# Kernel tuning notes

Hardware: AMD Instinct MI355X
Metric: run time of the kernel (lower is better)

## Reference

```python
import jax, jax.numpy as jnp
import numpy as np

N = 50000      # nodes (cells)
E = 800000     # directed edges
IN, H1, H2, Z = 512, 128, 128, 64


def setup_inputs() -> dict:
    key = jax.random.key(0)
    ks = jax.random.split(key, 12)
    x = jax.random.normal(ks[0], (N, IN), jnp.float32)
    edge_index = jax.random.randint(ks[1], (2, E), 0, N, dtype=jnp.int64)

    def glorot(k, i, o):
        return jax.random.normal(k, (i, o), jnp.float32) * np.float32(1.0 / np.sqrt(i))

    return {
        "x": x,
        "edge_index": edge_index,
        "W1": glorot(ks[2], IN, H1), "b1": jnp.zeros((H1,), jnp.float32),
        "W2": glorot(ks[3], H1, H2), "b2": jnp.zeros((H2,), jnp.float32),
        "Wm": glorot(ks[4], H2, Z),  "bm": jnp.zeros((Z,), jnp.float32),
        "Ws": glorot(ks[5], H2, Z),  "bs": jnp.zeros((Z,), jnp.float32),
    }


def _gcn_norm(edge_index, n):
    # PyG GCNConv default: add self-loops, sym-normalize D^-1/2 (A+I) D^-1/2
    loops = jnp.arange(n, dtype=edge_index.dtype)
    src = jnp.concatenate([edge_index[0], loops])
    dst = jnp.concatenate([edge_index[1], loops])
    deg = jax.ops.segment_sum(jnp.ones_like(dst, jnp.float32), dst, num_segments=n)
    dis = jnp.where(deg > 0, jax.lax.rsqrt(jnp.maximum(deg, 1.0)), 0.0)
    norm = dis[src] * dis[dst]  # [E+N]
    return src, dst, norm


def _gcn_conv(x, W, b, src, dst, norm, n):
    h = x @ W                          # [N, out] transform first
    msg = h[src] * norm[:, None]       # gather + scale
    out = jax.ops.segment_sum(msg, dst, num_segments=n)  # scatter-add at targets
    return out + b


def reference(x, edge_index, W1, b1, W2, b2, Wm, bm, Ws, bs):
    n = x.shape[0]
    src, dst, norm = _gcn_norm(edge_index, n)
    h = jax.nn.relu(_gcn_conv(x, W1, b1, src, dst, norm, n))
    h = jax.nn.relu(_gcn_conv(h, W2, b2, src, dst, norm, n))
    # dropout p=0.4 is identity in eval mode
    z_mean = _gcn_conv(h, Wm, bm, src, dst, norm, n)
    z_log_std = _gcn_conv(h, Ws, bs, src, dst, norm, n)
    return (z_mean, z_log_std)
```

## Files before the change

kernel.cpp:

```cpp
#include <hip/hip_runtime.h>


using u16 = unsigned short;
typedef __attribute__((ext_vector_type(8))) short short8;
typedef __attribute__((ext_vector_type(4))) float f32x4;

__device__ __forceinline__ void split_bf16(float f, u16& hi, u16& lo) {
    unsigned b = __float_as_uint(f);
    hi = (u16)(b >> 16);
    float rem = f - __uint_as_float(b & 0xFFFF0000u);
    lo = (u16)(__float_as_uint(rem) >> 16);
}

__device__ __forceinline__ int block_mode(const int* __restrict__ ew, int* sflag) {
    if (threadIdx.x == 0) *sflag = 0;
    __syncthreads();
    if (ew[2 * (int)threadIdx.x + 1] != 0) atomicOr(sflag, 1);
    __syncthreads();
    return *sflag ? 0 : 1;
}

__global__ void deg_kernel(const int* __restrict__ ew, int* __restrict__ deg, int E) {
    __shared__ int sflag;
    int mode = block_mode(ew, &sflag);
    int e = blockIdx.x * blockDim.x + threadIdx.x;
    if (e >= E) return;
    int d = mode ? ew[2 * E + 2 * e] : ew[E + e];
    atomicAdd(&deg[d], 1);
}

__global__ void scan_block_kernel(const int* __restrict__ deg, int* __restrict__ rowptr,
                                  int* __restrict__ aux, float* __restrict__ dis, int N) {
    __shared__ int s[256];
    int i = blockIdx.x * 256 + threadIdx.x;
    int v = (i < N) ? deg[i] : 0;
    if (i < N) dis[i] = rsqrtf((float)v + 1.0f);
    s[threadIdx.x] = v;
    __syncthreads();
    for (int off = 1; off < 256; off <<= 1) {
        int t = (threadIdx.x >= off) ? s[threadIdx.x - off] : 0;
        __syncthreads();
        s[threadIdx.x] += t;
        __syncthreads();
    }
    if (i < N) rowptr[i] = s[threadIdx.x] - v;
    if (threadIdx.x == 255) aux[blockIdx.x] = s[255];
}

__global__ void scan_aux_kernel(int* __restrict__ aux, int nb) {
    __shared__ int s[256];
    int i = threadIdx.x;
    int v = (i < nb) ? aux[i] : 0;
    s[i] = v;
    __syncthreads();
    for (int off = 1; off < 256; off <<= 1) {
        int t = (i >= off) ? s[i - off] : 0;
        __syncthreads();
        s[i] += t;
        __syncthreads();
    }
    if (i < nb) aux[i] = s[i] - v;
}

__global__ void add_offsets_kernel(int* __restrict__ rowptr, const int* __restrict__ aux,
                                   int* __restrict__ cursor, int N, int E) {
    int i = blockIdx.x * 256 + threadIdx.x;
    if (i < N) {
        int rp = rowptr[i] + aux[i >> 8];
        rowptr[i] = rp;
        cursor[i] = rp;
    }
    if (i == 0) rowptr[N] = E;
}

__global__ void fill_csr_kernel(const int* __restrict__ ew,
                                int* __restrict__ cursor,
                                int* __restrict__ csr_src, int E) {
    __shared__ int sflag;
    int mode = block_mode(ew, &sflag);
    int e = blockIdx.x * blockDim.x + threadIdx.x;
    if (e >= E) return;
    int s = mode ? ew[2 * e] : ew[e];
    int d = mode ? ew[2 * E + 2 * e] : ew[E + e];
    int pos = atomicAdd(&cursor[d], 1);
    csr_src[pos] = s;
}

__global__ void conv_all_kernel(const float* __restrict__ W1, const float* __restrict__ W2,
                                const float* __restrict__ Wm, const float* __restrict__ Ws,
                                u16* __restrict__ B1h, u16* __restrict__ B1l,
                                u16* __restrict__ B2h, u16* __restrict__ B2l,
                                u16* __restrict__ Bch, u16* __restrict__ Bcl) {
    int idx = blockIdx.x * 256 + threadIdx.x;
    u16 h, l;
    if (idx < 65536) {
        int t = idx >> 13;
        int ks = (idx >> 9) & 15;
        int L = (idx >> 3) & 63;
        int q = idx & 7;
        int col = t * 16 + (L & 15);
        int k = ks * 32 + (L >> 4) * 8 + q;
        split_bf16(W1[k * 128 + col], h, l);
        B1h[idx] = h;
        B1l[idx] = l;
    } else if (idx < 81920) {
        int o = idx - 65536;
        int t = o >> 11;
        int ks = (o >> 9) & 3;
        int L = (o >> 3) & 63;
        int q = o & 7;
        int col = t * 16 + (L & 15);
        int k = ks * 32 + (L >> 4) * 8 + q;
        split_bf16(W2[k * 128 + col], h, l);
        B2h[o] = h;
        B2l[o] = l;
    } else if (idx < 98304) {
        int o = idx - 81920;
        int t = o >> 11;
        int ks = (o >> 9) & 3;
        int L = (o >> 3) & 63;
        int q = o & 7;
        int col = t * 16 + (L & 15);
        int k = ks * 32 + (L >> 4) * 8 + q;
        float f = (col < 64) ? Wm[k * 64 + col] : Ws[k * 64 + (col - 64)];
        split_bf16(f, h, l);
        Bch[o] = h;
        Bcl[o] = l;
    }
}

#define TILE_OFF(t) ((t) * 520)

__global__ __launch_bounds__(256) void gemm_mfma(const float* __restrict__ A,
                                                 const u16* __restrict__ Bfh,
                                                 const u16* __restrict__ Bfl,
                                                 const float* __restrict__ dis,
                                                 float* __restrict__ C,
                                                 int N, int K) {
    __shared__ __align__(16) u16 AsH[4 * 520], AsL[4 * 520];

    const int tid = threadIdx.x;
    const int w = tid >> 6, lane = tid & 63;
    const int m16 = lane & 15, quad = lane >> 4;
    const int row0 = blockIdx.x * 64;

    const int s_ar = w * 16 + (lane & 15);
    const int s_ak = (lane >> 4) * 8;
    const int a_dst = TILE_OFF(w) + lane * 8;

    const int R = (w >> 1) * 32, Cc = (w & 1) * 64;
    const int atile = (w >> 1) * 2;
    const int btile = (w & 1) * 4;

    const int ksteps = K >> 5;
    const u16* bfh = Bfh + ((size_t)btile * ksteps) * 512 + lane * 8;
    const u16* bfl = Bfl + ((size_t)btile * ksteps) * 512 + lane * 8;

    f32x4 acc[2][4];
#pragma unroll
    for (int i = 0; i < 2; ++i)
#pragma unroll
        for (int j = 0; j < 4; ++j) acc[i][j] = (f32x4)0.f;

    float dr[2][4];
#pragma unroll
    for (int i = 0; i < 2; ++i)
#pragma unroll
        for (int r = 0; r < 4; ++r) {
            int gr = row0 + R + i * 16 + quad * 4 + r;
            dr[i][r] = dis[gr < N ? gr : N - 1];
        }

    const int grow = row0 + s_ar;
    const bool ok = (grow < N);
    const float* aptr = A + (size_t)grow * K + s_ak;

    float av[8];
    {
        f32x4 v0 = (f32x4)0.f, v1 = (f32x4)0.f;
        if (ok) { v0 = *(const f32x4*)&aptr[0]; v1 = *(const f32x4*)&aptr[4]; }
#pragma unroll
        for (int q = 0; q < 4; ++q) { av[q] = v0[q]; av[4 + q] = v1[q]; }
    }

    for (int ks = 0; ks < ksteps; ++ks) {
        short8 fbh[4], fbl[4];
#pragma unroll
        for (int j = 0; j < 4; ++j) {
            fbh[j] = *(const short8*)(bfh + (size_t)(j * ksteps + ks) * 512);
            fbl[j] = *(const short8*)(bfl + (size_t)(j * ksteps + ks) * 512);
        }

        short8 ah, al;
#pragma unroll
        for (int q = 0; q < 8; ++q) {
            u16 h, l;
            split_bf16(av[q], h, l);
            ah[q] = (short)h;
            al[q] = (short)l;
        }
        __syncthreads();
        *(short8*)&AsH[a_dst] = ah;
        *(short8*)&AsL[a_dst] = al;
        __syncthreads();

        if (ks + 1 < ksteps) {
            const int k0 = (ks + 1) * 32;
            f32x4 v0 = (f32x4)0.f, v1 = (f32x4)0.f;
            if (ok) { v0 = *(const f32x4*)&aptr[k0]; v1 = *(const f32x4*)&aptr[k0 + 4]; }
#pragma unroll
            for (int q = 0; q < 4; ++q) { av[q] = v0[q]; av[4 + q] = v1[q]; }
        }

        short8 fah[2], fal[2];
#pragma unroll
        for (int i = 0; i < 2; ++i) {
            fah[i] = *(const short8*)&AsH[TILE_OFF(atile + i) + lane * 8];
            fal[i] = *(const short8*)&AsL[TILE_OFF(atile + i) + lane * 8];
        }

#pragma unroll
        for (int i = 0; i < 2; ++i)
#pragma unroll
            for (int j = 0; j < 4; ++j) {
                acc[i][j] = __builtin_amdgcn_mfma_f32_16x16x32_bf16(
                    fah[i], fbh[j], acc[i][j], 0, 0, 0);
                acc[i][j] = __builtin_amdgcn_mfma_f32_16x16x32_bf16(
                    fah[i], fbl[j], acc[i][j], 0, 0, 0);
                acc[i][j] = __builtin_amdgcn_mfma_f32_16x16x32_bf16(
                    fal[i], fbh[j], acc[i][j], 0, 0, 0);
            }
    }

#pragma unroll
    for (int i = 0; i < 2; ++i) {
#pragma unroll
        for (int r = 0; r < 4; ++r) {
            int gr = row0 + R + i * 16 + quad * 4 + r;
            if (gr < N) {
#pragma unroll
                for (int j = 0; j < 4; ++j)
                    C[(size_t)gr * 128 + Cc + j * 16 + m16] = acc[i][j][r] * dr[i][r];
            }
        }
    }
}

__global__ __launch_bounds__(256) void propagate_kernel(
    const float* __restrict__ hs, const int* __restrict__ rowptr,
    const int* __restrict__ csr_src, const float* __restrict__ dis,
    const float* __restrict__ bias, float* __restrict__ out, int N, int do_relu) {
    int wave = (blockIdx.x * 256 + threadIdx.x) >> 6;
    int lane = threadIdx.x & 63;
    if (wave >= N) return;
    const int v = wave;
    const int half = lane >> 5, c = lane & 31;
    const int f4 = c * 4;
    const float dv = dis[v];
    f32x4 acc = (f32x4)0.f;
    const int beg = rowptr[v], end = rowptr[v + 1];
    int i = beg;
    for (; i + 8 <= end; i += 8) {
        int s[4];
        f32x4 g[4];
#pragma unroll
        for (int u = 0; u < 4; ++u) s[u] = csr_src[i + 2 * u + half];
#pragma unroll
        for (int u = 0; u < 4; ++u) g[u] = *(const f32x4*)&hs[(size_t)s[u] * 128 + f4];
#pragma unroll
        for (int u = 0; u < 4; ++u) acc += g[u];
    }
    for (; i + 2 <= end; i += 2) {
        int s = csr_src[i + half];
        acc += *(const f32x4*)&hs[(size_t)s * 128 + f4];
    }
    if (i < end && half == 0) {
        int s = csr_src[i];
        acc += *(const f32x4*)&hs[(size_t)s * 128 + f4];
    }
#pragma unroll
    for (int k = 0; k < 4; ++k) acc[k] += __shfl_xor(acc[k], 32);
    if (half == 0) {
        const f32x4 hv = *(const f32x4*)&hs[(size_t)v * 128 + f4];
        const f32x4 b = *(const f32x4*)&bias[f4];
        f32x4 o;
#pragma unroll
        for (int k = 0; k < 4; ++k) {
            float t = dv * (acc[k] + hv[k]) + b[k];
            o[k] = do_relu ? fmaxf(t, 0.f) : t;
        }
        *(f32x4*)&out[(size_t)v * 128 + f4] = o;
    }
}

__global__ void __launch_bounds__(256) propagate_final_kernel(
    const float* __restrict__ hs, const int* __restrict__ rowptr,
    const int* __restrict__ csr_src, const float* __restrict__ dis,
    const float* __restrict__ bm, const float* __restrict__ bs,
    float* __restrict__ out, int N) {
    int wave = (blockIdx.x * 256 + threadIdx.x) >> 6;
    int lane = threadIdx.x & 63;
    if (wave >= N) return;
    const int v = wave;
    const int half = lane >> 5, c = lane & 31;
    const int f4 = c * 4;
    const float dv = dis[v];
    f32x4 acc = (f32x4)0.f;
    const int beg = rowptr[v], end = rowptr[v + 1];
    int i = beg;
    for (; i + 8 <= end; i += 8) {
        int s[4];
        f32x4 g[4];
#pragma unroll
        for (int u = 0; u < 4; ++u) s[u] = csr_src[i + 2 * u + half];
#pragma unroll
        for (int u = 0; u < 4; ++u) g[u] = *(const f32x4*)&hs[(size_t)s[u] * 128 + f4];
#pragma unroll
        for (int u = 0; u < 4; ++u) acc += g[u];
    }
    for (; i + 2 <= end; i += 2) {
        int s = csr_src[i + half];
        acc += *(const f32x4*)&hs[(size_t)s * 128 + f4];
    }
    if (i < end && half == 0) {
        int s = csr_src[i];
        acc += *(const f32x4*)&hs[(size_t)s * 128 + f4];
    }
#pragma unroll
    for (int k = 0; k < 4; ++k) acc[k] += __shfl_xor(acc[k], 32);
    if (half == 0) {
        const f32x4 hv = *(const f32x4*)&hs[(size_t)v * 128 + f4];
        f32x4 o;
        if (f4 < 64) {
            const f32x4 b = *(const f32x4*)&bm[f4];
#pragma unroll
            for (int k = 0; k < 4; ++k) o[k] = dv * (acc[k] + hv[k]) + b[k];
            *(f32x4*)&out[(size_t)v * 64 + f4] = o;
        } else {
            const int g = f4 - 64;
            const f32x4 b = *(const f32x4*)&bs[g];
#pragma unroll
            for (int k = 0; k < 4; ++k) o[k] = dv * (acc[k] + hv[k]) + b[k];
            *(f32x4*)&out[(size_t)N * 64 + (size_t)v * 64 + g] = o;
        }
    }
}

extern "C" void kernel_launch(void* const* d_in, const int* in_sizes, int n_in,
                              void* d_out, int out_size, void* d_ws, size_t ws_size,
                              hipStream_t stream) {
    const float* x  = (const float*)d_in[0];
    const int*   ew = (const int*)d_in[1];
    const float* W1 = (const float*)d_in[2];
    const float* b1 = (const float*)d_in[3];
    const float* W2 = (const float*)d_in[4];
    const float* b2 = (const float*)d_in[5];
    const float* Wm = (const float*)d_in[6];
    const float* bm = (const float*)d_in[7];
    const float* Ws = (const float*)d_in[8];
    const float* bs = (const float*)d_in[9];
    float* out = (float*)d_out;

    const int IN = 512, H = 128;
    const int N = in_sizes[0] / IN;
    const int E = in_sizes[1] / 2;

    char* base = (char*)d_ws;
    size_t off = 0;
    auto alloc = [&](size_t bytes) -> char* {
        char* p = base + off;
        off = (off + bytes + 255) & ~(size_t)255;
        return p;
    };
    int*   deg     = (int*)  alloc((size_t)N * 4);
    int*   cursor  = (int*)  alloc((size_t)N * 4);
    float* dis     = (float*)alloc((size_t)N * 4);
    int*   rowptr  = (int*)  alloc((size_t)(N + 1) * 4);
    int*   aux     = (int*)  alloc(256 * 4);
    int*   csr_src = (int*)  alloc((size_t)E * 4);
    u16*   B1h     = (u16*)  alloc((size_t)IN * H * 2);
    u16*   B1l     = (u16*)  alloc((size_t)IN * H * 2);
    u16*   B2h     = (u16*)  alloc((size_t)H * H * 2);
    u16*   B2l     = (u16*)  alloc((size_t)H * H * 2);
    u16*   Bch     = (u16*)  alloc((size_t)H * H * 2);
    u16*   Bcl     = (u16*)  alloc((size_t)H * H * 2);
    float* hA      = (float*)alloc((size_t)N * H * 4);
    float* hB      = (float*)alloc((size_t)N * H * 4);
    (void)ws_size; (void)n_in; (void)out_size;

    hipMemsetAsync(deg, 0, (size_t)N * 4, stream);

    const int eblocks = (E + 255) / 256;
    const int nblocks = (N + 255) / 256;

    conv_all_kernel<<<(98304 + 255) / 256, 256, 0, stream>>>(
        W1, W2, Wm, Ws, B1h, B1l, B2h, B2l, Bch, Bcl);
    deg_kernel<<<eblocks, 256, 0, stream>>>(ew, deg, E);
    scan_block_kernel<<<nblocks, 256, 0, stream>>>(deg, rowptr, aux, dis, N);
    scan_aux_kernel<<<1, 256, 0, stream>>>(aux, nblocks);
    add_offsets_kernel<<<nblocks, 256, 0, stream>>>(rowptr, aux, cursor, N, E);
    fill_csr_kernel<<<eblocks, 256, 0, stream>>>(ew, cursor, csr_src, E);

    const int gblocks = (N + 63) / 64;
    const int pblocks = (N * 64 + 255) / 256;

    gemm_mfma<<<gblocks, 256, 0, stream>>>(x, B1h, B1l, dis, hA, N, IN);
    propagate_kernel<<<pblocks, 256, 0, stream>>>(hA, rowptr, csr_src, dis,
                                                  b1, hB, N, 1);
    gemm_mfma<<<gblocks, 256, 0, stream>>>(hB, B2h, B2l, dis, hA, N, H);
    propagate_kernel<<<pblocks, 256, 0, stream>>>(hA, rowptr, csr_src, dis,
                                                  b2, hB, N, 1);
    gemm_mfma<<<gblocks, 256, 0, stream>>>(hB, Bch, Bcl, dis, hA, N, H);
    propagate_final_kernel<<<pblocks, 256, 0, stream>>>(hA, rowptr, csr_src, dis,
                                                        bm, bs, out, N);
}
```

Measured before the change: 488.0 us.

## Fuse all stages into one persistent kernel with software grid barriers

Replaces the chain of eleven kernel launches (weight conversion, degree count, scans, CSR fill, three GEMMs, three propagations) with one persistent kernel of 768 blocks. The stages are separated by an atomic counter and generation grid barrier, and the work is spread with grid-stride loops. This removes per-launch overhead and the idle gaps between kernels. In exchange it relies on all 768 blocks being resident at once (launch_bounds 256,3), otherwise the barrier deadlocks. It also adds spin-wait barrier cost and may cut per-stage occupancy and parallelism compared with the full-size grids.

```diff
diff --git a/kernel.cpp b/kernel.cpp
--- a/kernel.cpp
+++ b/kernel.cpp
@@ -12,137 +12,33 @@
     lo = (u16)(__float_as_uint(rem) >> 16);
 }
 
-__device__ __forceinline__ int block_mode(const int* __restrict__ ew, int* sflag) {
-    if (threadIdx.x == 0) *sflag = 0;
+#define TILE_OFF(t) ((t) * 520)
+
+__device__ __forceinline__ void gbar(int* cnt, int* gen, int nb) {
     __syncthreads();
-    if (ew[2 * (int)threadIdx.x + 1] != 0) atomicOr(sflag, 1);
+    if (threadIdx.x == 0) {
+        __threadfence();
+        int g = atomicAdd(gen, 0);
+        if (atomicAdd(cnt, 1) == nb - 1) {
+            atomicExch(cnt, 0);
+            atomicAdd(gen, 1);
+        } else {
+            while (atomicAdd(gen, 0) == g) __builtin_amdgcn_s_sleep(2);
+        }
+        __threadfence();
+    }
     __syncthreads();
-    return *sflag ? 0 : 1;
-}
-
-__global__ void deg_kernel(const int* __restrict__ ew, int* __restrict__ deg, int E) {
-    __shared__ int sflag;
-    int mode = block_mode(ew, &sflag);
-    int e = blockIdx.x * blockDim.x + threadIdx.x;
-    if (e >= E) return;
-    int d = mode ? ew[2 * E + 2 * e] : ew[E + e];
-    atomicAdd(&deg[d], 1);
-}
-
-__global__ void scan_block_kernel(const int* __restrict__ deg, int* __restrict__ rowptr,
-                                  int* __restrict__ aux, float* __restrict__ dis, int N) {
-    __shared__ int s[256];
-    int i = blockIdx.x * 256 + threadIdx.x;
-    int v = (i < N) ? deg[i] : 0;
-    if (i < N) dis[i] = rsqrtf((float)v + 1.0f);
-    s[threadIdx.x] = v;
-    __syncthreads();
-    for (int off = 1; off < 256; off <<= 1) {
-        int t = (threadIdx.x >= off) ? s[threadIdx.x - off] : 0;
-        __syncthreads();
-        s[threadIdx.x] += t;
-        __syncthreads();
-    }
-    if (i < N) rowptr[i] = s[threadIdx.x] - v;
-    if (threadIdx.x == 255) aux[blockIdx.x] = s[255];
-}
-
-__global__ void scan_aux_kernel(int* __restrict__ aux, int nb) {
-    __shared__ int s[256];
-    int i = threadIdx.x;
-    int v = (i < nb) ? aux[i] : 0;
-    s[i] = v;
-    __syncthreads();
-    for (int off = 1; off < 256; off <<= 1) {
-        int t = (i >= off) ? s[i - off] : 0;
-        __syncthreads();
-        s[i] += t;
-        __syncthreads();
-    }
-    if (i < nb) aux[i] = s[i] - v;
-}
-
-__global__ void add_offsets_kernel(int* __restrict__ rowptr, const int* __restrict__ aux,
-                                   int* __restrict__ cursor, int N, int E) {
-    int i = blockIdx.x * 256 + threadIdx.x;
-    if (i < N) {
-        int rp = rowptr[i] + aux[i >> 8];
-        rowptr[i] = rp;
-        cursor[i] = rp;
-    }
-    if (i == 0) rowptr[N] = E;
-}
-
-__global__ void fill_csr_kernel(const int* __restrict__ ew,
-                                int* __restrict__ cursor,
-                                int* __restrict__ csr_src, int E) {
-    __shared__ int sflag;
-    int mode = block_mode(ew, &sflag);
-    int e = blockIdx.x * blockDim.x + threadIdx.x;
-    if (e >= E) return;
-    int s = mode ? ew[2 * e] : ew[e];
-    int d = mode ? ew[2 * E + 2 * e] : ew[E + e];
-    int pos = atomicAdd(&cursor[d], 1);
-    csr_src[pos] = s;
-}
-
-__global__ void conv_all_kernel(const float* __restrict__ W1, const float* __restrict__ W2,
-                                const float* __restrict__ Wm, const float* __restrict__ Ws,
-                                u16* __restrict__ B1h, u16* __restrict__ B1l,
-                                u16* __restrict__ B2h, u16* __restrict__ B2l,
-                                u16* __restrict__ Bch, u16* __restrict__ Bcl) {
-    int idx = blockIdx.x * 256 + threadIdx.x;
-    u16 h, l;
-    if (idx < 65536) {
-        int t = idx >> 13;
-        int ks = (idx >> 9) & 15;
-        int L = (idx >> 3) & 63;
-        int q = idx & 7;
-        int col = t * 16 + (L & 15);
-        int k = ks * 32 + (L >> 4) * 8 + q;
-        split_bf16(W1[k * 128 + col], h, l);
-        B1h[idx] = h;
-        B1l[idx] = l;
-    } else if (idx < 81920) {
-        int o = idx - 65536;
-        int t = o >> 11;
-        int ks = (o >> 9) & 3;
-        int L = (o >> 3) & 63;
-        int q = o & 7;
-        int col = t * 16 + (L & 15);
-        int k = ks * 32 + (L >> 4) * 8 + q;
-        split_bf16(W2[k * 128 + col], h, l);
-        B2h[o] = h;
-        B2l[o] = l;
-    } else if (idx < 98304) {
-        int o = idx - 81920;
-        int t = o >> 11;
-        int ks = (o >> 9) & 3;
-        int L = (o >> 3) & 63;
-        int q = o & 7;
-        int col = t * 16 + (L & 15);
-        int k = ks * 32 + (L >> 4) * 8 + q;
-        float f = (col < 64) ? Wm[k * 64 + col] : Ws[k * 64 + (col - 64)];
-        split_bf16(f, h, l);
-        Bch[o] = h;
-        Bcl[o] = l;
-    }
-}
-
-#define TILE_OFF(t) ((t) * 520)
-
-__global__ __launch_bounds__(256) void gemm_mfma(const float* __restrict__ A,
-                                                 const u16* __restrict__ Bfh,
-                                                 const u16* __restrict__ Bfl,
-                                                 const float* __restrict__ dis,
-                                                 float* __restrict__ C,
-                                                 int N, int K) {
-    __shared__ __align__(16) u16 AsH[4 * 520], AsL[4 * 520];
-
+}
+
+__device__ __forceinline__ void gemm_tile(
+    const float* __restrict__ A, const u16* __restrict__ Bfh,
+    const u16* __restrict__ Bfl, const float* __restrict__ dis,
+    float* __restrict__ C, int N, int K, int tile,
+    u16* AsH, u16* AsL) {
     const int tid = threadIdx.x;
     const int w = tid >> 6, lane = tid & 63;
     const int m16 = lane & 15, quad = lane >> 4;
-    const int row0 = blockIdx.x * 64;
+    const int row0 = tile * 64;
 
     const int s_ar = w * 16 + (lane & 15);
     const int s_ak = (lane >> 4) * 8;
@@ -246,104 +142,239 @@
     }
 }
 
-__global__ __launch_bounds__(256) void propagate_kernel(
+__device__ __forceinline__ void prop_std(
     const float* __restrict__ hs, const int* __restrict__ rowptr,
     const int* __restrict__ csr_src, const float* __restrict__ dis,
-    const float* __restrict__ bias, float* __restrict__ out, int N, int do_relu) {
-    int wave = (blockIdx.x * 256 + threadIdx.x) >> 6;
-    int lane = threadIdx.x & 63;
-    if (wave >= N) return;
-    const int v = wave;
+    const float* __restrict__ bias, float* __restrict__ o, int N,
+    int do_relu, int nwaves) {
+    const int lane = threadIdx.x & 63;
     const int half = lane >> 5, c = lane & 31;
     const int f4 = c * 4;
-    const float dv = dis[v];
-    f32x4 acc = (f32x4)0.f;
-    const int beg = rowptr[v], end = rowptr[v + 1];
-    int i = beg;
-    for (; i + 8 <= end; i += 8) {
-        int s[4];
-        f32x4 g[4];
-#pragma unroll
-        for (int u = 0; u < 4; ++u) s[u] = csr_src[i + 2 * u + half];
-#pragma unroll
-        for (int u = 0; u < 4; ++u) g[u] = *(const f32x4*)&hs[(size_t)s[u] * 128 + f4];
-#pragma unroll
-        for (int u = 0; u < 4; ++u) acc += g[u];
-    }
-    for (; i + 2 <= end; i += 2) {
-        int s = csr_src[i + half];
-        acc += *(const f32x4*)&hs[(size_t)s * 128 + f4];
-    }
-    if (i < end && half == 0) {
-        int s = csr_src[i];
-        acc += *(const f32x4*)&hs[(size_t)s * 128 + f4];
-    }
-#pragma unroll
-    for (int k = 0; k < 4; ++k) acc[k] += __shfl_xor(acc[k], 32);
-    if (half == 0) {
-        const f32x4 hv = *(const f32x4*)&hs[(size_t)v * 128 + f4];
-        const f32x4 b = *(const f32x4*)&bias[f4];
-        f32x4 o;
-#pragma unroll
-        for (int k = 0; k < 4; ++k) {
-            float t = dv * (acc[k] + hv[k]) + b[k];
-            o[k] = do_relu ? fmaxf(t, 0.f) : t;
-        }
-        *(f32x4*)&out[(size_t)v * 128 + f4] = o;
-    }
-}
-
-__global__ void __launch_bounds__(256) propagate_final_kernel(
+    const int w0 = ((int)blockIdx.x * 256 + (int)threadIdx.x) >> 6;
+    for (int v = w0; v < N; v += nwaves) {
+        const float dv = dis[v];
+        f32x4 acc = (f32x4)0.f;
+        const int beg = rowptr[v], end = rowptr[v + 1];
+        int i = beg;
+        for (; i + 8 <= end; i += 8) {
+            int s[4];
+            f32x4 g[4];
+#pragma unroll
+            for (int u = 0; u < 4; ++u) s[u] = csr_src[i + 2 * u + half];
+#pragma unroll
+            for (int u = 0; u < 4; ++u) g[u] = *(const f32x4*)&hs[(size_t)s[u] * 128 + f4];
+#pragma unroll
+            for (int u = 0; u < 4; ++u) acc += g[u];
+        }
+        for (; i + 2 <= end; i += 2) {
+            int s = csr_src[i + half];
+            acc += *(const f32x4*)&hs[(size_t)s * 128 + f4];
+        }
+        if (i < end && half == 0) {
+            int s = csr_src[i];
+            acc += *(const f32x4*)&hs[(size_t)s * 128 + f4];
+        }
+#pragma unroll
+        for (int k = 0; k < 4; ++k) acc[k] += __shfl_xor(acc[k], 32);
+        if (half == 0) {
+            const f32x4 hv = *(const f32x4*)&hs[(size_t)v * 128 + f4];
+            const f32x4 b = *(const f32x4*)&bias[f4];
+            f32x4 oo;
+#pragma unroll
+            for (int k = 0; k < 4; ++k) {
+                float t = dv * (acc[k] + hv[k]) + b[k];
+                oo[k] = do_relu ? fmaxf(t, 0.f) : t;
+            }
+            *(f32x4*)&o[(size_t)v * 128 + f4] = oo;
+        }
+    }
+}
+
+__device__ __forceinline__ void prop_fin(
     const float* __restrict__ hs, const int* __restrict__ rowptr,
     const int* __restrict__ csr_src, const float* __restrict__ dis,
     const float* __restrict__ bm, const float* __restrict__ bs,
-    float* __restrict__ out, int N) {
-    int wave = (blockIdx.x * 256 + threadIdx.x) >> 6;
-    int lane = threadIdx.x & 63;
-    if (wave >= N) return;
-    const int v = wave;
+    float* __restrict__ o, int N, int nwaves) {
+    const int lane = threadIdx.x & 63;
     const int half = lane >> 5, c = lane & 31;
     const int f4 = c * 4;
-    const float dv = dis[v];
-    f32x4 acc = (f32x4)0.f;
-    const int beg = rowptr[v], end = rowptr[v + 1];
-    int i = beg;
-    for (; i + 8 <= end; i += 8) {
-        int s[4];
-        f32x4 g[4];
-#pragma unroll
-        for (int u = 0; u < 4; ++u) s[u] = csr_src[i + 2 * u + half];
-#pragma unroll
-        for (int u = 0; u < 4; ++u) g[u] = *(const f32x4*)&hs[(size_t)s[u] * 128 + f4];
-#pragma unroll
-        for (int u = 0; u < 4; ++u) acc += g[u];
-    }
-    for (; i + 2 <= end; i += 2) {
-        int s = csr_src[i + half];
-        acc += *(const f32x4*)&hs[(size_t)s * 128 + f4];
-    }
-    if (i < end && half == 0) {
-        int s = csr_src[i];
-        acc += *(const f32x4*)&hs[(size_t)s * 128 + f4];
-    }
-#pragma unroll
-    for (int k = 0; k < 4; ++k) acc[k] += __shfl_xor(acc[k], 32);
-    if (half == 0) {
-        const f32x4 hv = *(const f32x4*)&hs[(size_t)v * 128 + f4];
-        f32x4 o;
-        if (f4 < 64) {
-            const f32x4 b = *(const f32x4*)&bm[f4];
-#pragma unroll
-            for (int k = 0; k < 4; ++k) o[k] = dv * (acc[k] + hv[k]) + b[k];
-            *(f32x4*)&out[(size_t)v * 64 + f4] = o;
+    const int w0 = ((int)blockIdx.x * 256 + (int)threadIdx.x) >> 6;
+    for (int v = w0; v < N; v += nwaves) {
+        const float dv = dis[v];
+        f32x4 acc = (f32x4)0.f;
+        const int beg = rowptr[v], end = rowptr[v + 1];
+        int i = beg;
+        for (; i + 8 <= end; i += 8) {
+            int s[4];
+            f32x4 g[4];
+#pragma unroll
+            for (int u = 0; u < 4; ++u) s[u] = csr_src[i + 2 * u + half];
+#pragma unroll
+            for (int u = 0; u < 4; ++u) g[u] = *(const f32x4*)&hs[(size_t)s[u] * 128 + f4];
+#pragma unroll
+            for (int u = 0; u < 4; ++u) acc += g[u];
+        }
+        for (; i + 2 <= end; i += 2) {
+            int s = csr_src[i + half];
+            acc += *(const f32x4*)&hs[(size_t)s * 128 + f4];
+        }
+        if (i < end && half == 0) {
+            int s = csr_src[i];
+            acc += *(const f32x4*)&hs[(size_t)s * 128 + f4];
+        }
+#pragma unroll
+        for (int k = 0; k < 4; ++k) acc[k] += __shfl_xor(acc[k], 32);
+        if (half == 0) {
+            const f32x4 hv = *(const f32x4*)&hs[(size_t)v * 128 + f4];
+            f32x4 oo;
+            if (f4 < 64) {
+                const f32x4 b = *(const f32x4*)&bm[f4];
+#pragma unroll
+                for (int k = 0; k < 4; ++k) oo[k] = dv * (acc[k] + hv[k]) + b[k];
+                *(f32x4*)&o[(size_t)v * 64 + f4] = oo;
+            } else {
+                const int g = f4 - 64;
+                const f32x4 b = *(const f32x4*)&bs[g];
+#pragma unroll
+                for (int k = 0; k < 4; ++k) oo[k] = dv * (acc[k] + hv[k]) + b[k];
+                *(f32x4*)&o[(size_t)N * 64 + (size_t)v * 64 + g] = oo;
+            }
+        }
+    }
+}
+
+__global__ __launch_bounds__(256, 3) void fused_all(
+    const float* __restrict__ x, const int* __restrict__ ew,
+    const float* __restrict__ W1, const float* __restrict__ b1,
+    const float* __restrict__ W2, const float* __restrict__ b2,
+    const float* __restrict__ Wm, const float* __restrict__ bm,
+    const float* __restrict__ Ws, const float* __restrict__ bs,
+    int* cnt, int* gen, int* deg, int* cursor, float* dis,
+    int* rowptr, int* aux, int* csr_src,
+    u16* B1h, u16* B1l, u16* B2h, u16* B2l, u16* Bch, u16* Bcl,
+    float* hA, float* hB, float* out, int N, int E) {
+    __shared__ __align__(16) u16 AsH[4 * 520], AsL[4 * 520];
+    __shared__ int sint[257];
+
+    const int tid = threadIdx.x;
+    const int bid = blockIdx.x;
+    const int NB = gridDim.x;
+    const int gtid = bid * 256 + tid;
+    const int GT = NB * 256;
+    const int nwaves = NB * 4;
+
+    int mode;
+    {
+        if (tid == 0) sint[256] = 0;
+        __syncthreads();
+        if (ew[2 * tid + 1] != 0) atomicOr(&sint[256], 1);
+        __syncthreads();
+        mode = sint[256] ? 0 : 1;
+        __syncthreads();
+    }
+
+    if (gtid < 98304) {
+        int idx = gtid;
+        u16 h, l;
+        if (idx < 65536) {
+            int t = idx >> 13, ks = (idx >> 9) & 15, L = (idx >> 3) & 63, q = idx & 7;
+            int col = t * 16 + (L & 15);
+            int k = ks * 32 + (L >> 4) * 8 + q;
+            split_bf16(W1[k * 128 + col], h, l);
+            B1h[idx] = h; B1l[idx] = l;
+        } else if (idx < 81920) {
+            int o = idx - 65536;
+            int t = o >> 11, ks = (o >> 9) & 3, L = (o >> 3) & 63, q = o & 7;
+            int col = t * 16 + (L & 15);
+            int k = ks * 32 + (L >> 4) * 8 + q;
+            split_bf16(W2[k * 128 + col], h, l);
+            B2h[o] = h; B2l[o] = l;
         } else {
-            const int g = f4 - 64;
-            const f32x4 b = *(const f32x4*)&bs[g];
-#pragma unroll
-            for (int k = 0; k < 4; ++k) o[k] = dv * (acc[k] + hv[k]) + b[k];
-            *(f32x4*)&out[(size_t)N * 64 + (size_t)v * 64 + g] = o;
-        }
-    }
+            int o = idx - 81920;
+            int t = o >> 11, ks = (o >> 9) & 3, L = (o >> 3) & 63, q = o & 7;
+            int col = t * 16 + (L & 15);
+            int k = ks * 32 + (L >> 4) * 8 + q;
+            float f = (col < 64) ? Wm[k * 64 + col] : Ws[k * 64 + (col - 64)];
+            split_bf16(f, h, l);
+            Bch[o] = h; Bcl[o] = l;
+        }
+    }
+    for (int e = gtid; e < E; e += GT) {
+        int d = mode ? ew[2 * E + 2 * e] : ew[E + e];
+        atomicAdd(&deg[d], 1);
+    }
+    gbar(cnt, gen, NB);
+
+    const int nch = (N + 255) >> 8;
+    for (int ch = bid; ch < nch; ch += NB) {
+        int i = ch * 256 + tid;
+        int v = (i < N) ? deg[i] : 0;
+        if (i < N) dis[i] = rsqrtf((float)v + 1.0f);
+        sint[tid] = v;
+        __syncthreads();
+        for (int off = 1; off < 256; off <<= 1) {
+            int t = (tid >= off) ? sint[tid - off] : 0;
+            __syncthreads();
+            sint[tid] += t;
+            __syncthreads();
+        }
+        if (i < N) rowptr[i] = sint[tid] - v;
+        if (tid == 255) aux[ch] = sint[255];
+        __syncthreads();
+    }
+    gbar(cnt, gen, NB);
+
+    if (bid == 0) {
+        int v = (tid < nch) ? aux[tid] : 0;
+        sint[tid] = v;
+        __syncthreads();
+        for (int off = 1; off < 256; off <<= 1) {
+            int t = (tid >= off) ? sint[tid - off] : 0;
+            __syncthreads();
+            sint[tid] += t;
+            __syncthreads();
+        }
+        if (tid < nch) aux[tid] = sint[tid] - v;
+    }
+    gbar(cnt, gen, NB);
+
+    for (int i = gtid; i < N; i += GT) {
+        int rp = rowptr[i] + aux[i >> 8];
+        rowptr[i] = rp;
+        cursor[i] = rp;
+    }
+    if (gtid == 0) rowptr[N] = E;
+    gbar(cnt, gen, NB);
+
+    for (int e = gtid; e < E; e += GT) {
+        int s = mode ? ew[2 * e] : ew[e];
+        int d = mode ? ew[2 * E + 2 * e] : ew[E + e];
+        int pos = atomicAdd(&cursor[d], 1);
+        csr_src[pos] = s;
+    }
+    gbar(cnt, gen, NB);
+
+    const int ntiles = (N + 63) >> 6;
+
+    for (int t = bid; t < ntiles; t += NB)
+        gemm_tile(x, B1h, B1l, dis, hA, N, 512, t, AsH, AsL);
+    gbar(cnt, gen, NB);
+
+    prop_std(hA, rowptr, csr_src, dis, b1, hB, N, 1, nwaves);
+    gbar(cnt, gen, NB);
+
+    for (int t = bid; t < ntiles; t += NB)
+        gemm_tile(hB, B2h, B2l, dis, hA, N, 128, t, AsH, AsL);
+    gbar(cnt, gen, NB);
+
+    prop_std(hA, rowptr, csr_src, dis, b2, hB, N, 1, nwaves);
+    gbar(cnt, gen, NB);
+
+    for (int t = bid; t < ntiles; t += NB)
+        gemm_tile(hB, Bch, Bcl, dis, hA, N, 128, t, AsH, AsL);
+    gbar(cnt, gen, NB);
+
+    prop_fin(hA, rowptr, csr_src, dis, bm, bs, out, N, nwaves);
 }
 
 extern "C" void kernel_launch(void* const* d_in, const int* in_sizes, int n_in,
@@ -372,6 +403,7 @@
         off = (off + bytes + 255) & ~(size_t)255;
         return p;
     };
+    int*   sync2   = (int*)  alloc(256);
     int*   deg     = (int*)  alloc((size_t)N * 4);
     int*   cursor  = (int*)  alloc((size_t)N * 4);
     float* dis     = (float*)alloc((size_t)N * 4);
@@ -388,29 +420,11 @@
     float* hB      = (float*)alloc((size_t)N * H * 4);
     (void)ws_size; (void)n_in; (void)out_size;
 
-    hipMemsetAsync(deg, 0, (size_t)N * 4, stream);
-
-    const int eblocks = (E + 255) / 256;
-    const int nblocks = (N + 255) / 256;
-
-    conv_all_kernel<<<(98304 + 255) / 256, 256, 0, stream>>>(
-        W1, W2, Wm, Ws, B1h, B1l, B2h, B2l, Bch, Bcl);
-    deg_kernel<<<eblocks, 256, 0, stream>>>(ew, deg, E);
-    scan_block_kernel<<<nblocks, 256, 0, stream>>>(deg, rowptr, aux, dis, N);
-    scan_aux_kernel<<<1, 256, 0, stream>>>(aux, nblocks);
-    add_offsets_kernel<<<nblocks, 256, 0, stream>>>(rowptr, aux, cursor, N, E);
-    fill_csr_kernel<<<eblocks, 256, 0, stream>>>(ew, cursor, csr_src, E);
-
-    const int gblocks = (N + 63) / 64;
-    const int pblocks = (N * 64 + 255) / 256;
-
-    gemm_mfma<<<gblocks, 256, 0, stream>>>(x, B1h, B1l, dis, hA, N, IN);
-    propagate_kernel<<<pblocks, 256, 0, stream>>>(hA, rowptr, csr_src, dis,
-                                                  b1, hB, N, 1);
-    gemm_mfma<<<gblocks, 256, 0, stream>>>(hB, B2h, B2l, dis, hA, N, H);
-    propagate_kernel<<<pblocks, 256, 0, stream>>>(hA, rowptr, csr_src, dis,
-                                                  b2, hB, N, 1);
-    gemm_mfma<<<gblocks, 256, 0, stream>>>(hB, Bch, Bcl, dis, hA, N, H);
-    propagate_final_kernel<<<pblocks, 256, 0, stream>>>(hA, rowptr, csr_src, dis,
-                                                        bm, bs, out, N);
-}
+    size_t zlen = (size_t)((char*)cursor - (char*)sync2);
+    hipMemsetAsync(sync2, 0, zlen, stream);
+
+    fused_all<<<768, 256, 0, stream>>>(
+        x, ew, W1, b1, W2, b2, Wm, bm, Ws, bs,
+        &sync2[0], &sync2[1], deg, cursor, dis, rowptr, aux, csr_src,
+        B1h, B1l, B2h, B2l, Bch, Bcl, hA, hB, out, N, E);
+}
```

New measurement: 1.353 ms. 177% more time.

## Fuse preprocessing kernels and overlap CSR fill with first GEMM

Applied to the files above, without the earlier changes.

Merges weight conversion with degree counting into one launch, and folds the auxiliary scan into the offset-add kernel so each block rescans the block sums itself. Runs the CSR fill as extra blocks of the first GEMM launch, since the layer-1 GEMM only needs the degree-based normalisation and not the CSR. This removes three launches and lets the atomic-heavy scatter overlap the MFMA work. The cost is a redundant per-block scan and heterogeneous blocks inside one grid.

```diff
diff --git a/kernel.cpp b/kernel.cpp
--- a/kernel.cpp
+++ b/kernel.cpp
@@ -11,6 +11,8 @@
     float rem = f - __uint_as_float(b & 0xFFFF0000u);
     lo = (u16)(__float_as_uint(rem) >> 16);
 }
+
+#define TILE_OFF(t) ((t) * 520)
 
 __device__ __forceinline__ int block_mode(const int* __restrict__ ew, int* sflag) {
     if (threadIdx.x == 0) *sflag = 0;
@@ -20,13 +22,158 @@
     return *sflag ? 0 : 1;
 }
 
-__global__ void deg_kernel(const int* __restrict__ ew, int* __restrict__ deg, int E) {
+__device__ __forceinline__ void gemm_tile(
+    const float* __restrict__ A, const u16* __restrict__ Bfh,
+    const u16* __restrict__ Bfl, const float* __restrict__ dis,
+    float* __restrict__ C, int N, int K, int tile,
+    u16* AsH, u16* AsL) {
+    const int tid = threadIdx.x;
+    const int w = tid >> 6, lane = tid & 63;
+    const int m16 = lane & 15, quad = lane >> 4;
+    const int row0 = tile * 64;
+
+    const int s_ar = w * 16 + (lane & 15);
+    const int s_ak = (lane >> 4) * 8;
+    const int a_dst = TILE_OFF(w) + lane * 8;
+
+    const int R = (w >> 1) * 32, Cc = (w & 1) * 64;
+    const int atile = (w >> 1) * 2;
+    const int btile = (w & 1) * 4;
+
+    const int ksteps = K >> 5;
+    const u16* bfh = Bfh + ((size_t)btile * ksteps) * 512 + lane * 8;
+    const u16* bfl = Bfl + ((size_t)btile * ksteps) * 512 + lane * 8;
+
+    f32x4 acc[2][4];
+#pragma unroll
+    for (int i = 0; i < 2; ++i)
+#pragma unroll
+        for (int j = 0; j < 4; ++j) acc[i][j] = (f32x4)0.f;
+
+    float dr[2][4];
+#pragma unroll
+    for (int i = 0; i < 2; ++i)
+#pragma unroll
+        for (int r = 0; r < 4; ++r) {
+            int gr = row0 + R + i * 16 + quad * 4 + r;
+            dr[i][r] = dis[gr < N ? gr : N - 1];
+        }
+
+    const int grow = row0 + s_ar;
+    const bool ok = (grow < N);
+    const float* aptr = A + (size_t)grow * K + s_ak;
+
+    float av[8];
+    {
+        f32x4 v0 = (f32x4)0.f, v1 = (f32x4)0.f;
+        if (ok) { v0 = *(const f32x4*)&aptr[0]; v1 = *(const f32x4*)&aptr[4]; }
+#pragma unroll
+        for (int q = 0; q < 4; ++q) { av[q] = v0[q]; av[4 + q] = v1[q]; }
+    }
+
+    for (int ks = 0; ks < ksteps; ++ks) {
+        short8 fbh[4], fbl[4];
+#pragma unroll
+        for (int j = 0; j < 4; ++j) {
+            fbh[j] = *(const short8*)(bfh + (size_t)(j * ksteps + ks) * 512);
+            fbl[j] = *(const short8*)(bfl + (size_t)(j * ksteps + ks) * 512);
+        }
+
+        short8 ah, al;
+#pragma unroll
+        for (int q = 0; q < 8; ++q) {
+            u16 h, l;
+            split_bf16(av[q], h, l);
+            ah[q] = (short)h;
+            al[q] = (short)l;
+        }
+        __syncthreads();
+        *(short8*)&AsH[a_dst] = ah;
+        *(short8*)&AsL[a_dst] = al;
+        __syncthreads();
+
+        if (ks + 1 < ksteps) {
+            const int k0 = (ks + 1) * 32;
+            f32x4 v0 = (f32x4)0.f, v1 = (f32x4)0.f;
+            if (ok) { v0 = *(const f32x4*)&aptr[k0]; v1 = *(const f32x4*)&aptr[k0 + 4]; }
+#pragma unroll
+            for (int q = 0; q < 4; ++q) { av[q] = v0[q]; av[4 + q] = v1[q]; }
+        }
+
+        short8 fah[2], fal[2];
+#pragma unroll
+        for (int i = 0; i < 2; ++i) {
+            fah[i] = *(const short8*)&AsH[TILE_OFF(atile + i) + lane * 8];
+            fal[i] = *(const short8*)&AsL[TILE_OFF(atile + i) + lane * 8];
+        }
+
+#pragma unroll
+        for (int i = 0; i < 2; ++i)
+#pragma unroll
+            for (int j = 0; j < 4; ++j) {
+                acc[i][j] = __builtin_amdgcn_mfma_f32_16x16x32_bf16(
+                    fah[i], fbh[j], acc[i][j], 0, 0, 0);
+                acc[i][j] = __builtin_amdgcn_mfma_f32_16x16x32_bf16(
+                    fah[i], fbl[j], acc[i][j], 0, 0, 0);
+                acc[i][j] = __builtin_amdgcn_mfma_f32_16x16x32_bf16(
+                    fal[i], fbh[j], acc[i][j], 0, 0, 0);
+            }
+    }
+
+#pragma unroll
+    for (int i = 0; i < 2; ++i) {
+#pragma unroll
+        for (int r = 0; r < 4; ++r) {
+            int gr = row0 + R + i * 16 + quad * 4 + r;
+            if (gr < N) {
+#pragma unroll
+                for (int j = 0; j < 4; ++j)
+                    C[(size_t)gr * 128 + Cc + j * 16 + m16] = acc[i][j][r] * dr[i][r];
+            }
+        }
+    }
+}
+
+__global__ void conv_deg_kernel(
+    const float* __restrict__ W1, const float* __restrict__ W2,
+    const float* __restrict__ Wm, const float* __restrict__ Ws,
+    u16* __restrict__ B1h, u16* __restrict__ B1l,
+    u16* __restrict__ B2h, u16* __restrict__ B2l,
+    u16* __restrict__ Bch, u16* __restrict__ Bcl,
+    const int* __restrict__ ew, int* __restrict__ deg, int E) {
     __shared__ int sflag;
     int mode = block_mode(ew, &sflag);
-    int e = blockIdx.x * blockDim.x + threadIdx.x;
-    if (e >= E) return;
-    int d = mode ? ew[2 * E + 2 * e] : ew[E + e];
-    atomicAdd(&deg[d], 1);
+    int gtid = blockIdx.x * 256 + threadIdx.x;
+    if (gtid < 98304) {
+        int idx = gtid;
+        u16 h, l;
+        if (idx < 65536) {
+            int t = idx >> 13, ks = (idx >> 9) & 15, L = (idx >> 3) & 63, q = idx & 7;
+            int col = t * 16 + (L & 15);
+            int k = ks * 32 + (L >> 4) * 8 + q;
+            split_bf16(W1[k * 128 + col], h, l);
+            B1h[idx] = h; B1l[idx] = l;
+        } else if (idx < 81920) {
+            int o = idx - 65536;
+            int t = o >> 11, ks = (o >> 9) & 3, L = (o >> 3) & 63, q = o & 7;
+            int col = t * 16 + (L & 15);
+            int k = ks * 32 + (L >> 4) * 8 + q;
+            split_bf16(W2[k * 128 + col], h, l);
+            B2h[o] = h; B2l[o] = l;
+        } else {
+            int o = idx - 81920;
+            int t = o >> 11, ks = (o >> 9) & 3, L = (o >> 3) & 63, q = o & 7;
+            int col = t * 16 + (L & 15);
+            int k = ks * 32 + (L >> 4) * 8 + q;
+            float f = (col < 64) ? Wm[k * 64 + col] : Ws[k * 64 + (col - 64)];
+            split_bf16(f, h, l);
+            Bch[o] = h; Bcl[o] = l;
+        }
+    }
+    if (gtid < E) {
+        int d = mode ? ew[2 * E + 2 * gtid] : ew[E + gtid];
+        atomicAdd(&deg[d], 1);
+    }
 }
 
 __global__ void scan_block_kernel(const int* __restrict__ deg, int* __restrict__ rowptr,
@@ -47,89 +194,50 @@
     if (threadIdx.x == 255) aux[blockIdx.x] = s[255];
 }
 
-__global__ void scan_aux_kernel(int* __restrict__ aux, int nb) {
+__global__ void offsets_kernel(int* __restrict__ rowptr, const int* __restrict__ aux,
+                               int* __restrict__ cursor, int N, int E, int nch) {
     __shared__ int s[256];
-    int i = threadIdx.x;
-    int v = (i < nb) ? aux[i] : 0;
-    s[i] = v;
+    const int b = blockIdx.x, tid = threadIdx.x;
+    int v = (tid < nch) ? aux[tid] : 0;
+    s[tid] = v;
     __syncthreads();
     for (int off = 1; off < 256; off <<= 1) {
-        int t = (i >= off) ? s[i - off] : 0;
-        __syncthreads();
-        s[i] += t;
-        __syncthreads();
-    }
-    if (i < nb) aux[i] = s[i] - v;
-}
-
-__global__ void add_offsets_kernel(int* __restrict__ rowptr, const int* __restrict__ aux,
-                                   int* __restrict__ cursor, int N, int E) {
-    int i = blockIdx.x * 256 + threadIdx.x;
+        int t = (tid >= off) ? s[tid - off] : 0;
+        __syncthreads();
+        s[tid] += t;
+        __syncthreads();
+    }
+    const int excl = (b == 0) ? 0 : s[b - 1];
+    int i = b * 256 + tid;
     if (i < N) {
-        int rp = rowptr[i] + aux[i >> 8];
+        int rp = rowptr[i] + excl;
         rowptr[i] = rp;
         cursor[i] = rp;
     }
-    if (i == 0) rowptr[N] = E;
-}
-
-__global__ void fill_csr_kernel(const int* __restrict__ ew,
-                                int* __restrict__ cursor,
-                                int* __restrict__ csr_src, int E) {
+    if (b == 0 && tid == 0) rowptr[N] = E;
+}
+
+__global__ __launch_bounds__(256) void gemm1_fill_kernel(
+    const float* __restrict__ A, const u16* __restrict__ Bfh,
+    const u16* __restrict__ Bfl, const float* __restrict__ dis,
+    float* __restrict__ C, int N, int gtiles,
+    const int* __restrict__ ew, int* __restrict__ cursor,
+    int* __restrict__ csr_src, int E) {
+    __shared__ __align__(16) u16 AsH[4 * 520], AsL[4 * 520];
     __shared__ int sflag;
-    int mode = block_mode(ew, &sflag);
-    int e = blockIdx.x * blockDim.x + threadIdx.x;
-    if (e >= E) return;
-    int s = mode ? ew[2 * e] : ew[e];
-    int d = mode ? ew[2 * E + 2 * e] : ew[E + e];
-    int pos = atomicAdd(&cursor[d], 1);
-    csr_src[pos] = s;
-}
-
-__global__ void conv_all_kernel(const float* __restrict__ W1, const float* __restrict__ W2,
-                                const float* __restrict__ Wm, const float* __restrict__ Ws,
-                                u16* __restrict__ B1h, u16* __restrict__ B1l,
-                                u16* __restrict__ B2h, u16* __restrict__ B2l,
-                                u16* __restrict__ Bch, u16* __restrict__ Bcl) {
-    int idx = blockIdx.x * 256 + threadIdx.x;
-    u16 h, l;
-    if (idx < 65536) {
-        int t = idx >> 13;
-        int ks = (idx >> 9) & 15;
-        int L = (idx >> 3) & 63;
-        int q = idx & 7;
-        int col = t * 16 + (L & 15);
-        int k = ks * 32 + (L >> 4) * 8 + q;
-        split_bf16(W1[k * 128 + col], h, l);
-        B1h[idx] = h;
-        B1l[idx] = l;
-    } else if (idx < 81920) {
-        int o = idx - 65536;
-        int t = o >> 11;
-        int ks = (o >> 9) & 3;
-        int L = (o >> 3) & 63;
-        int q = o & 7;
-        int col = t * 16 + (L & 15);
-        int k = ks * 32 + (L >> 4) * 8 + q;
-        split_bf16(W2[k * 128 + col], h, l);
-        B2h[o] = h;
-        B2l[o] = l;
-    } else if (idx < 98304) {
-        int o = idx - 81920;
-        int t = o >> 11;
-        int ks = (o >> 9) & 3;
-        int L = (o >> 3) & 63;
-        int q = o & 7;
-        int col = t * 16 + (L & 15);
-        int k = ks * 32 + (L >> 4) * 8 + q;
-        float f = (col < 64) ? Wm[k * 64 + col] : Ws[k * 64 + (col - 64)];
-        split_bf16(f, h, l);
-        Bch[o] = h;
-        Bcl[o] = l;
-    }
-}
-
-#define TILE_OFF(t) ((t) * 520)
+    if ((int)blockIdx.x < gtiles) {
+        gemm_tile(A, Bfh, Bfl, dis, C, N, 512, blockIdx.x, AsH, AsL);
+    } else {
+        int mode = block_mode(ew, &sflag);
+        int e = ((int)blockIdx.x - gtiles) * 256 + (int)threadIdx.x;
+        if (e < E) {
+            int s = mode ? ew[2 * e] : ew[e];
+            int d = mode ? ew[2 * E + 2 * e] : ew[E + e];
+            int pos = atomicAdd(&cursor[d], 1);
+            csr_src[pos] = s;
+        }
+    }
+}
 
 __global__ __launch_bounds__(256) void gemm_mfma(const float* __restrict__ A,
                                                  const u16* __restrict__ Bfh,
@@ -138,112 +246,7 @@
                                                  float* __restrict__ C,
                                                  int N, int K) {
     __shared__ __align__(16) u16 AsH[4 * 520], AsL[4 * 520];
-
-    const int tid = threadIdx.x;
-    const int w = tid >> 6, lane = tid & 63;
-    const int m16 = lane & 15, quad = lane >> 4;
-    const int row0 = blockIdx.x * 64;
-
-    const int s_ar = w * 16 + (lane & 15);
-    const int s_ak = (lane >> 4) * 8;
-    const int a_dst = TILE_OFF(w) + lane * 8;
-
-    const int R = (w >> 1) * 32, Cc = (w & 1) * 64;
-    const int atile = (w >> 1) * 2;
-    const int btile = (w & 1) * 4;
-
-    const int ksteps = K >> 5;
-    const u16* bfh = Bfh + ((size_t)btile * ksteps) * 512 + lane * 8;
-    const u16* bfl = Bfl + ((size_t)btile * ksteps) * 512 + lane * 8;
-
-    f32x4 acc[2][4];
-#pragma unroll
-    for (int i = 0; i < 2; ++i)
-#pragma unroll
-        for (int j = 0; j < 4; ++j) acc[i][j] = (f32x4)0.f;
-
-    float dr[2][4];
-#pragma unroll
-    for (int i = 0; i < 2; ++i)
-#pragma unroll
-        for (int r = 0; r < 4; ++r) {
-            int gr = row0 + R + i * 16 + quad * 4 + r;
-            dr[i][r] = dis[gr < N ? gr : N - 1];
-        }
-
-    const int grow = row0 + s_ar;
-    const bool ok = (grow < N);
-    const float* aptr = A + (size_t)grow * K + s_ak;
-
-    float av[8];
-    {
-        f32x4 v0 = (f32x4)0.f, v1 = (f32x4)0.f;
-        if (ok) { v0 = *(const f32x4*)&aptr[0]; v1 = *(const f32x4*)&aptr[4]; }
-#pragma unroll
-        for (int q = 0; q < 4; ++q) { av[q] = v0[q]; av[4 + q] = v1[q]; }
-    }
-
-    for (int ks = 0; ks < ksteps; ++ks) {
-        short8 fbh[4], fbl[4];
-#pragma unroll
-        for (int j = 0; j < 4; ++j) {
-            fbh[j] = *(const short8*)(bfh + (size_t)(j * ksteps + ks) * 512);
-            fbl[j] = *(const short8*)(bfl + (size_t)(j * ksteps + ks) * 512);
-        }
-
-        short8 ah, al;
-#pragma unroll
-        for (int q = 0; q < 8; ++q) {
-            u16 h, l;
-            split_bf16(av[q], h, l);
-            ah[q] = (short)h;
-            al[q] = (short)l;
-        }
-        __syncthreads();
-        *(short8*)&AsH[a_dst] = ah;
-        *(short8*)&AsL[a_dst] = al;
-        __syncthreads();
-
-        if (ks + 1 < ksteps) {
-            const int k0 = (ks + 1) * 32;
-            f32x4 v0 = (f32x4)0.f, v1 = (f32x4)0.f;
-            if (ok) { v0 = *(const f32x4*)&aptr[k0]; v1 = *(const f32x4*)&aptr[k0 + 4]; }
-#pragma unroll
-            for (int q = 0; q < 4; ++q) { av[q] = v0[q]; av[4 + q] = v1[q]; }
-        }
-
-        short8 fah[2], fal[2];
-#pragma unroll
-        for (int i = 0; i < 2; ++i) {
-            fah[i] = *(const short8*)&AsH[TILE_OFF(atile + i) + lane * 8];
-            fal[i] = *(const short8*)&AsL[TILE_OFF(atile + i) + lane * 8];
-        }
-
-#pragma unroll
-        for (int i = 0; i < 2; ++i)
-#pragma unroll
-            for (int j = 0; j < 4; ++j) {
-                acc[i][j] = __builtin_amdgcn_mfma_f32_16x16x32_bf16(
-                    fah[i], fbh[j], acc[i][j], 0, 0, 0);
-                acc[i][j] = __builtin_amdgcn_mfma_f32_16x16x32_bf16(
-                    fah[i], fbl[j], acc[i][j], 0, 0, 0);
-                acc[i][j] = __builtin_amdgcn_mfma_f32_16x16x32_bf16(
-                    fal[i], fbh[j], acc[i][j], 0, 0, 0);
-            }
-    }
-
-#pragma unroll
-    for (int i = 0; i < 2; ++i) {
-#pragma unroll
-        for (int r = 0; r < 4; ++r) {
-            int gr = row0 + R + i * 16 + quad * 4 + r;
-            if (gr < N) {
-#pragma unroll
-                for (int j = 0; j < 4; ++j)
-                    C[(size_t)gr * 128 + Cc + j * 16 + m16] = acc[i][j][r] * dr[i][r];
-            }
-        }
-    }
+    gemm_tile(A, Bfh, Bfl, dis, C, N, K, blockIdx.x, AsH, AsL);
 }
 
 __global__ __launch_bounds__(256) void propagate_kernel(
@@ -392,25 +395,22 @@
 
     const int eblocks = (E + 255) / 256;
     const int nblocks = (N + 255) / 256;
-
-    conv_all_kernel<<<(98304 + 255) / 256, 256, 0, stream>>>(
-        W1, W2, Wm, Ws, B1h, B1l, B2h, B2l, Bch, Bcl);
-    deg_kernel<<<eblocks, 256, 0, stream>>>(ew, deg, E);
+    const int nch = nblocks;
+    const int gtiles = (N + 63) / 64;
+    const int pblocks = (N * 64 + 255) / 256;
+
+    conv_deg_kernel<<<eblocks, 256, 0, stream>>>(
+        W1, W2, Wm, Ws, B1h, B1l, B2h, B2l, Bch, Bcl, ew, deg, E);
     scan_block_kernel<<<nblocks, 256, 0, stream>>>(deg, rowptr, aux, dis, N);
-    scan_aux_kernel<<<1, 256, 0, stream>>>(aux, nblocks);
-    add_offsets_kernel<<<nblocks, 256, 0, stream>>>(rowptr, aux, cursor, N, E);
-    fill_csr_kernel<<<eblocks, 256, 0, stream>>>(ew, cursor, csr_src, E);
-
-    const int gblocks = (N + 63) / 64;
-    const int pblocks = (N * 64 + 255) / 256;
-
-    gemm_mfma<<<gblocks, 256, 0, stream>>>(x, B1h, B1l, dis, hA, N, IN);
+    offsets_kernel<<<nblocks, 256, 0, stream>>>(rowptr, aux, cursor, N, E, nch);
+    gemm1_fill_kernel<<<gtiles + eblocks, 256, 0, stream>>>(
+        x, B1h, B1l, dis, hA, N, gtiles, ew, cursor, csr_src, E);
     propagate_kernel<<<pblocks, 256, 0, stream>>>(hA, rowptr, csr_src, dis,
                                                   b1, hB, N, 1);
-    gemm_mfma<<<gblocks, 256, 0, stream>>>(hB, B2h, B2l, dis, hA, N, H);
+    gemm_mfma<<<gtiles, 256, 0, stream>>>(hB, B2h, B2l, dis, hA, N, H);
     propagate_kernel<<<pblocks, 256, 0, stream>>>(hA, rowptr, csr_src, dis,
                                                   b2, hB, N, 1);
-    gemm_mfma<<<gblocks, 256, 0, stream>>>(hB, Bch, Bcl, dis, hA, N, H);
+    gemm_mfma<<<gtiles, 256, 0, stream>>>(hB, Bch, Bcl, dis, hA, N, H);
     propagate_final_kernel<<<pblocks, 256, 0, stream>>>(hA, rowptr, csr_src, dis,
                                                         bm, bs, out, N);
 }
```

Result: faster. 451.8 us (-7.4%).
